# Optimization experiments

Hardware: AMD Instinct MI355X
Metric: run time of the kernel (lower is better)

Reference implementation:

```python
import math
import jax, jax.numpy as jnp
import numpy as np

K = 10          # hard-coded k in forward
ALPHA = 0.1
THETA = 0.5
BN_EPS = 1e-5


def setup_inputs() -> dict:
    key = jax.random.key(0)
    ks = jax.random.split(key, 8)
    B, N, H, L = 16, 4096, 128, 4
    s = lambda i, shp: jax.random.normal(ks[i], shp, jnp.float32) * 0.05
    return dict(
        pos=jax.random.normal(ks[0], (B, N, 3), jnp.float32),
        W0=s(1, (3, H)), b0=jnp.zeros((H,), jnp.float32),
        Wc=s(2, (L, H, H)),
        W1=s(3, (H, H)), b1=jnp.zeros((H,), jnp.float32),
        Wm1=s(4, (H, H)), bm1=jnp.zeros((H,), jnp.float32),
        g1=jnp.ones((H,), jnp.float32), be1=jnp.zeros((H,), jnp.float32),
        Wm2=s(5, (H, H)), bm2=jnp.zeros((H,), jnp.float32),
        g2=jnp.ones((H,), jnp.float32), be2=jnp.zeros((H,), jnp.float32),
        Wout=s(6, (H, 10)), bout=jnp.zeros((10,), jnp.float32),
    )


def _knn_idx(pos, k):
    # per-graph squared pairwise distances [B,N,N]; batch dim = graph id,
    # so no cross-graph edges (mirrors knn(x, x, k, batch, batch)).
    sq = jnp.sum(pos * pos, axis=-1)
    d2 = sq[:, :, None] + sq[:, None, :] - 2.0 * jnp.einsum('bnd,bmd->bnm', pos, pos)
    _, idx = jax.lax.top_k(-d2, k)  # [B,N,K], includes self (dist 0)
    return idx


def _bn_relu(x, g, b):
    # BatchNorm1d in training mode: batch statistics, biased variance
    mu = x.mean(0)
    var = x.var(0)
    return jax.nn.relu((x - mu) * jax.lax.rsqrt(var + BN_EPS) * g + b)


def _forward(pos, nbr, W0, b0, Wc, W1, b1, Wm1, bm1, g1, be1, Wm2, bm2, g2, be2, Wout, bout):
    x0 = jax.nn.relu(pos @ W0 + b0)                 # [B,N,H]
    x = x0
    gather = jax.vmap(lambda xb, nb: xb[nb])        # [B,N,K,H]
    for l in range(Wc.shape[0]):
        agg = gather(x, nbr).sum(axis=2)            # sum-aggregate, edge_weight = 1
        h = (1.0 - ALPHA) * agg + ALPHA * x0        # GCN2Conv initial residual
        beta = math.log(THETA / (l + 1) + 1.0)      # identity mapping strength
        x = jax.nn.relu((1.0 - beta) * h + beta * (h @ Wc[l]))
    x = x @ W1 + b1                                 # lins[1]
    pooled = x.max(axis=1)                          # global_max_pool -> [B,H]
    y = _bn_relu(pooled @ Wm1 + bm1, g1, be1)
    y = _bn_relu(y @ Wm2 + bm2, g2, be2)
    y = y @ Wout + bout
    return jax.nn.log_softmax(y, axis=-1)


def reference(pos, W0, b0, Wc, W1, b1, Wm1, bm1, g1, be1, Wm2, bm2, g2, be2, Wout, bout):
    nbr = _knn_idx(pos, K)  # index-only, non-differentiable (as in torch knn)
    return _forward(pos, nbr, W0, b0, Wc, W1, b1,
                    Wm1, bm1, g1, be1, Wm2, bm2, g2, be2, Wout, bout)
```

## Files before the change

kernel.cpp:

```cpp
#include <hip/hip_runtime.h>
#include <math.h>

#define NPTS 4096
#define HDIM 128
#define KNN 10
#define NSPLIT 4
#define CTILE 1024
#define SLOTS 12

__device__ __forceinline__ float relu_f(float x) { return x > 0.f ? x : 0.f; }
__device__ __forceinline__ float med3_f(float a, float b, float c) {
    return __builtin_amdgcn_fmed3f(a, b, c);
}

__global__ __launch_bounds__(256) void knn_part(const float* __restrict__ pos,
                                                uint2* __restrict__ pdi)
{
    __shared__ float4 spt[CTILE];
    const int bid = blockIdx.x;
    const int s = bid & 3;
    const int chunk = (bid >> 2) & 15;
    const int b = bid >> 6;
    const float* pb = pos + (size_t)b * NPTS * 3;
    const int c0 = s << 10;

    for (int j = threadIdx.x; j < CTILE; j += 256) {
        int g = c0 + j;
        float x = pb[3 * g + 0], y = pb[3 * g + 1], z = pb[3 * g + 2];
        float sq = __fadd_rn(__fadd_rn(__fmul_rn(x, x), __fmul_rn(y, y)), __fmul_rn(z, z));
        spt[j] = make_float4(x, y, z, sq);
    }
    __syncthreads();

    const int i = chunk * 256 + threadIdx.x;
    const float qx = pb[3 * i + 0], qy = pb[3 * i + 1], qz = pb[3 * i + 2];
    const float qw = __fadd_rn(__fadd_rn(__fmul_rn(qx, qx), __fmul_rn(qy, qy)), __fmul_rn(qz, qz));

    float bd[KNN];
#pragma unroll
    for (int m = 0; m < KNN; ++m) bd[m] = INFINITY;

#pragma unroll 4
    for (int j = 0; j < CTILE; ++j) {
        float4 p = spt[j];
        float dot = __fadd_rn(__fadd_rn(__fmul_rn(qx, p.x), __fmul_rn(qy, p.y)),
                              __fmul_rn(qz, p.z));
        float d2 = __fsub_rn(__fadd_rn(qw, p.w), __fmul_rn(2.f, dot));
#pragma unroll
        for (int m = KNN - 1; m > 0; --m) bd[m] = med3_f(d2, bd[m - 1], bd[m]);
        bd[0] = fminf(d2, bd[0]);
    }
    const float thr = bd[KNN - 1];

    uint2* o = pdi + ((size_t)(b * NPTS + i) * NSPLIT + s) * SLOTS;
    int cnt = 0;
#pragma unroll 4
    for (int j = 0; j < CTILE; ++j) {
        float4 p = spt[j];
        float dot = __fadd_rn(__fadd_rn(__fmul_rn(qx, p.x), __fmul_rn(qy, p.y)),
                              __fmul_rn(qz, p.z));
        float d2 = __fsub_rn(__fadd_rn(qw, p.w), __fmul_rn(2.f, dot));
        if (d2 <= thr && cnt < SLOTS) {
            o[cnt] = make_uint2(__float_as_uint(d2), (unsigned)(c0 + j));
            ++cnt;
        }
    }
}

__global__ __launch_bounds__(256) void knn_merge(const uint2* __restrict__ pdi,
                                                 int* __restrict__ nbr)
{
    const int q = blockIdx.x * 256 + threadIdx.x;
    const uint2* in = pdi + (size_t)q * (NSPLIT * SLOTS);
    float bd[KNN];
    int   bi[KNN];
#pragma unroll
    for (int m = 0; m < KNN; ++m) { bd[m] = 3.4e38f; bi[m] = 0; }
#pragma unroll
    for (int u = 0; u < NSPLIT * SLOTS; ++u) {
        uint2 v = in[u];
        float d2 = __uint_as_float(v.x);
        int   ix = (int)v.y;
        if (d2 < bd[KNN - 1]) {
            bool c[KNN];
#pragma unroll
            for (int m = 0; m < KNN; ++m) c[m] = d2 < bd[m];
#pragma unroll
            for (int m = KNN - 1; m > 0; --m) {
                bd[m] = c[m] ? (c[m - 1] ? bd[m - 1] : d2) : bd[m];
                bi[m] = c[m] ? (c[m - 1] ? bi[m - 1] : ix) : bi[m];
            }
            bd[0] = c[0] ? d2 : bd[0];
            bi[0] = c[0] ? ix : bi[0];
        }
    }
    const int b = q >> 12;
    int* o = nbr + (size_t)q * KNN;
#pragma unroll
    for (int m = 0; m < KNN; ++m) o[m] = (b << 12) + bi[m];
}

__global__ __launch_bounds__(256) void x0_kernel(const float* __restrict__ pos,
                                                 const float* __restrict__ W0,
                                                 const float* __restrict__ b0,
                                                 float* __restrict__ x0)
{
    int gid = blockIdx.x * 256 + threadIdx.x;
    int node = gid >> 5, qd = gid & 31;
    float px = pos[node * 3 + 0], py = pos[node * 3 + 1], pz = pos[node * 3 + 2];
    const float4 w0 = ((const float4*)W0)[qd];
    const float4 w1 = ((const float4*)W0)[32 + qd];
    const float4 w2 = ((const float4*)W0)[64 + qd];
    const float4 bb = ((const float4*)b0)[qd];
    float4 r;
    r.x = relu_f(fmaf(pz, w2.x, fmaf(py, w1.x, fmaf(px, w0.x, bb.x))));
    r.y = relu_f(fmaf(pz, w2.y, fmaf(py, w1.y, fmaf(px, w0.y, bb.y))));
    r.z = relu_f(fmaf(pz, w2.z, fmaf(py, w1.z, fmaf(px, w0.z, bb.z))));
    r.w = relu_f(fmaf(pz, w2.w, fmaf(py, w1.w, fmaf(px, w0.w, bb.w))));
    ((float4*)x0)[gid] = r;
}

__global__ __launch_bounds__(256) void gcn_layer(const float* __restrict__ xin,
                                                 float* __restrict__ xout,
                                                 const float* __restrict__ pos,
                                                 const float* __restrict__ W0,
                                                 const float* __restrict__ b0,
                                                 const float* __restrict__ Wl,
                                                 const int* __restrict__ nbr,
                                                 float omb, float beta)
{
    __shared__ float sh[64][129];
    __shared__ float sW[32 * 128];
    __shared__ float sW0[512];
    const int t = threadIdx.x;
    const int bid = blockIdx.x;
    const int swz = (bid & 7) * 128 + (bid >> 3);
    const int node0 = swz * 64;

    if (t < 128) {
        sW0[t] = W0[t]; sW0[128 + t] = W0[128 + t];
        sW0[256 + t] = W0[256 + t]; sW0[384 + t] = b0[t];
    }
    __syncthreads();

    const float4* xin4 = (const float4*)xin;
    for (int u = t; u < 64 * 32; u += 256) {
        int n = u >> 5, qd = u & 31;
        int node = node0 + n;
        float ax = 0.f, ay = 0.f, az = 0.f, aw = 0.f;
        const int* nb = nbr + node * KNN;
#pragma unroll
        for (int k = 0; k < KNN; ++k) {
            float4 v = xin4[nb[k] * 32 + qd];
            ax += v.x; ay += v.y; az += v.z; aw += v.w;
        }
        float px = pos[node * 3 + 0], py = pos[node * 3 + 1], pz = pos[node * 3 + 2];
        int c = qd * 4;
        sh[n][c + 0] = fmaf(0.9f, ax, 0.1f * relu_f(fmaf(pz, sW0[256 + c + 0], fmaf(py, sW0[128 + c + 0], fmaf(px, sW0[c + 0], sW0[384 + c + 0])))));
        sh[n][c + 1] = fmaf(0.9f, ay, 0.1f * relu_f(fmaf(pz, sW0[256 + c + 1], fmaf(py, sW0[128 + c + 1], fmaf(px, sW0[c + 1], sW0[384 + c + 1])))));
        sh[n][c + 2] = fmaf(0.9f, az, 0.1f * relu_f(fmaf(pz, sW0[256 + c + 2], fmaf(py, sW0[128 + c + 2], fmaf(px, sW0[c + 2], sW0[384 + c + 2])))));
        sh[n][c + 3] = fmaf(0.9f, aw, 0.1f * relu_f(fmaf(pz, sW0[256 + c + 3], fmaf(py, sW0[128 + c + 3], fmaf(px, sW0[c + 3], sW0[384 + c + 3])))));
    }

    const int rg = t >> 4;
    const int cq = t & 15;
    float acc[4][8];
#pragma unroll
    for (int r = 0; r < 4; ++r)
#pragma unroll
        for (int j = 0; j < 8; ++j) acc[r][j] = 0.f;

    const float4* W4 = (const float4*)Wl;
    for (int quarter = 0; quarter < 4; ++quarter) {
        __syncthreads();
        for (int u = t; u < 1024; u += 256) ((float4*)sW)[u] = W4[quarter * 1024 + u];
        __syncthreads();
#pragma unroll 4
        for (int ii = 0; ii < 32; ++ii) {
            int i = quarter * 32 + ii;
            float hv0 = sh[rg * 4 + 0][i];
            float hv1 = sh[rg * 4 + 1][i];
            float hv2 = sh[rg * 4 + 2][i];
            float hv3 = sh[rg * 4 + 3][i];
            const float4* row = (const float4*)(sW + ii * 128);
            float4 wA = row[cq];
            float4 wB = row[cq + 16];
            acc[0][0] = fmaf(hv0, wA.x, acc[0][0]); acc[0][1] = fmaf(hv0, wA.y, acc[0][1]);
            acc[0][2] = fmaf(hv0, wA.z, acc[0][2]); acc[0][3] = fmaf(hv0, wA.w, acc[0][3]);
            acc[0][4] = fmaf(hv0, wB.x, acc[0][4]); acc[0][5] = fmaf(hv0, wB.y, acc[0][5]);
            acc[0][6] = fmaf(hv0, wB.z, acc[0][6]); acc[0][7] = fmaf(hv0, wB.w, acc[0][7]);
            acc[1][0] = fmaf(hv1, wA.x, acc[1][0]); acc[1][1] = fmaf(hv1, wA.y, acc[1][1]);
            acc[1][2] = fmaf(hv1, wA.z, acc[1][2]); acc[1][3] = fmaf(hv1, wA.w, acc[1][3]);
            acc[1][4] = fmaf(hv1, wB.x, acc[1][4]); acc[1][5] = fmaf(hv1, wB.y, acc[1][5]);
            acc[1][6] = fmaf(hv1, wB.z, acc[1][6]); acc[1][7] = fmaf(hv1, wB.w, acc[1][7]);
            acc[2][0] = fmaf(hv2, wA.x, acc[2][0]); acc[2][1] = fmaf(hv2, wA.y, acc[2][1]);
            acc[2][2] = fmaf(hv2, wA.z, acc[2][2]); acc[2][3] = fmaf(hv2, wA.w, acc[2][3]);
            acc[2][4] = fmaf(hv2, wB.x, acc[2][4]); acc[2][5] = fmaf(hv2, wB.y, acc[2][5]);
            acc[2][6] = fmaf(hv2, wB.z, acc[2][6]); acc[2][7] = fmaf(hv2, wB.w, acc[2][7]);
            acc[3][0] = fmaf(hv3, wA.x, acc[3][0]); acc[3][1] = fmaf(hv3, wA.y, acc[3][1]);
            acc[3][2] = fmaf(hv3, wA.z, acc[3][2]); acc[3][3] = fmaf(hv3, wA.w, acc[3][3]);
            acc[3][4] = fmaf(hv3, wB.x, acc[3][4]); acc[3][5] = fmaf(hv3, wB.y, acc[3][5]);
            acc[3][6] = fmaf(hv3, wB.z, acc[3][6]); acc[3][7] = fmaf(hv3, wB.w, acc[3][7]);
        }
    }

#pragma unroll
    for (int r = 0; r < 4; ++r) {
        int row = rg * 4 + r;
        int node = node0 + row;
#pragma unroll
        for (int sel = 0; sel < 2; ++sel) {
            int c = cq * 4 + sel * 64;
            float4 o;
            o.x = relu_f(fmaf(omb, sh[row][c + 0], beta * acc[r][sel * 4 + 0]));
            o.y = relu_f(fmaf(omb, sh[row][c + 1], beta * acc[r][sel * 4 + 1]));
            o.z = relu_f(fmaf(omb, sh[row][c + 2], beta * acc[r][sel * 4 + 2]));
            o.w = relu_f(fmaf(omb, sh[row][c + 3], beta * acc[r][sel * 4 + 3]));
            ((float4*)(xout + (size_t)node * HDIM))[c >> 2] = o;
        }
    }
}

__global__ __launch_bounds__(256) void w1pool_kernel(const float* __restrict__ xin,
                                                     const float* __restrict__ W1,
                                                     const float* __restrict__ b1,
                                                     unsigned int* __restrict__ pool)
{
    __shared__ float sh[64][129];
    __shared__ float sW[32 * 128];
    __shared__ float smax[16][128];
    const int t = threadIdx.x;
    const int bid = blockIdx.x;
    const int swz = (bid & 7) * 128 + (bid >> 3);
    const int node0 = swz * 64;

    const float4* xin4 = (const float4*)xin;
    for (int u = t; u < 64 * 32; u += 256) {
        int n = u >> 5, qd = u & 31;
        float4 v = xin4[(node0 + n) * 32 + qd];
        int c = qd * 4;
        sh[n][c + 0] = v.x; sh[n][c + 1] = v.y; sh[n][c + 2] = v.z; sh[n][c + 3] = v.w;
    }

    const int rg = t >> 4;
    const int cq = t & 15;
    float acc[4][8];
#pragma unroll
    for (int r = 0; r < 4; ++r)
#pragma unroll
        for (int j = 0; j < 8; ++j) acc[r][j] = 0.f;

    const float4* W4 = (const float4*)W1;
    for (int quarter = 0; quarter < 4; ++quarter) {
        __syncthreads();
        for (int u = t; u < 1024; u += 256) ((float4*)sW)[u] = W4[quarter * 1024 + u];
        __syncthreads();
#pragma unroll 4
        for (int ii = 0; ii < 32; ++ii) {
            float hv0 = sh[rg * 4 + 0][quarter * 32 + ii];
            float hv1 = sh[rg * 4 + 1][quarter * 32 + ii];
            float hv2 = sh[rg * 4 + 2][quarter * 32 + ii];
            float hv3 = sh[rg * 4 + 3][quarter * 32 + ii];
            const float4* row = (const float4*)(sW + ii * 128);
            float4 wA = row[cq];
            float4 wB = row[cq + 16];
            acc[0][0] = fmaf(hv0, wA.x, acc[0][0]); acc[0][1] = fmaf(hv0, wA.y, acc[0][1]);
            acc[0][2] = fmaf(hv0, wA.z, acc[0][2]); acc[0][3] = fmaf(hv0, wA.w, acc[0][3]);
            acc[0][4] = fmaf(hv0, wB.x, acc[0][4]); acc[0][5] = fmaf(hv0, wB.y, acc[0][5]);
            acc[0][6] = fmaf(hv0, wB.z, acc[0][6]); acc[0][7] = fmaf(hv0, wB.w, acc[0][7]);
            acc[1][0] = fmaf(hv1, wA.x, acc[1][0]); acc[1][1] = fmaf(hv1, wA.y, acc[1][1]);
            acc[1][2] = fmaf(hv1, wA.z, acc[1][2]); acc[1][3] = fmaf(hv1, wA.w, acc[1][3]);
            acc[1][4] = fmaf(hv1, wB.x, acc[1][4]); acc[1][5] = fmaf(hv1, wB.y, acc[1][5]);
            acc[1][6] = fmaf(hv1, wB.z, acc[1][6]); acc[1][7] = fmaf(hv1, wB.w, acc[1][7]);
            acc[2][0] = fmaf(hv2, wA.x, acc[2][0]); acc[2][1] = fmaf(hv2, wA.y, acc[2][1]);
            acc[2][2] = fmaf(hv2, wA.z, acc[2][2]); acc[2][3] = fmaf(hv2, wA.w, acc[2][3]);
            acc[2][4] = fmaf(hv2, wB.x, acc[2][4]); acc[2][5] = fmaf(hv2, wB.y, acc[2][5]);
            acc[2][6] = fmaf(hv2, wB.z, acc[2][6]); acc[2][7] = fmaf(hv2, wB.w, acc[2][7]);
            acc[3][0] = fmaf(hv3, wA.x, acc[3][0]); acc[3][1] = fmaf(hv3, wA.y, acc[3][1]);
            acc[3][2] = fmaf(hv3, wA.z, acc[3][2]); acc[3][3] = fmaf(hv3, wA.w, acc[3][3]);
            acc[3][4] = fmaf(hv3, wB.x, acc[3][4]); acc[3][5] = fmaf(hv3, wB.y, acc[3][5]);
            acc[3][6] = fmaf(hv3, wB.z, acc[3][6]); acc[3][7] = fmaf(hv3, wB.w, acc[3][7]);
        }
    }

#pragma unroll
    for (int sel = 0; sel < 2; ++sel) {
#pragma unroll
        for (int j = 0; j < 4; ++j) {
            int c = cq * 4 + sel * 64 + j;
            float bc = b1[c];
            float m = acc[0][sel * 4 + j] + bc;
            m = fmaxf(m, acc[1][sel * 4 + j] + bc);
            m = fmaxf(m, acc[2][sel * 4 + j] + bc);
            m = fmaxf(m, acc[3][sel * 4 + j] + bc);
            smax[rg][c] = m;
        }
    }
    __syncthreads();
    if (t < 128) {
        float m = smax[0][t];
#pragma unroll
        for (int r = 1; r < 16; ++r) m = fmaxf(m, smax[r][t]);
        unsigned int u = __float_as_uint(m);
        unsigned int key = (u & 0x80000000u) ? ~u : (u | 0x80000000u);
        atomicMax(&pool[(node0 >> 12) * HDIM + t], key);
    }
}

__global__ __launch_bounds__(256) void head_kernel(const unsigned int* __restrict__ pool,
                                                   const float* __restrict__ Wm1, const float* __restrict__ bm1,
                                                   const float* __restrict__ g1,  const float* __restrict__ be1,
                                                   const float* __restrict__ Wm2, const float* __restrict__ bm2,
                                                   const float* __restrict__ g2,  const float* __restrict__ be2,
                                                   const float* __restrict__ Wout,const float* __restrict__ bout,
                                                   float* __restrict__ out)
{
    __shared__ float sA[16][128];
    __shared__ float sB[16][128];
    __shared__ float sL[16][10];
    const int t = threadIdx.x;
    for (int u = t; u < 2048; u += 256) {
        unsigned int k = pool[u];
        unsigned int orig = (k & 0x80000000u) ? (k ^ 0x80000000u) : ~k;
        sA[u >> 7][u & 127] = __uint_as_float(orig);
    }
    __syncthreads();

    if (t < 128) {
        float y[16];
#pragma unroll
        for (int b = 0; b < 16; ++b) y[b] = bm1[t];
        for (int i = 0; i < 128; ++i) {
            float w = Wm1[i * 128 + t];
#pragma unroll
            for (int b = 0; b < 16; ++b) y[b] = fmaf(sA[b][i], w, y[b]);
        }
        float mu = 0.f;
#pragma unroll
        for (int b = 0; b < 16; ++b) mu += y[b];
        mu *= (1.f / 16.f);
        float var = 0.f;
#pragma unroll
        for (int b = 0; b < 16; ++b) { float d = y[b] - mu; var = fmaf(d, d, var); }
        var *= (1.f / 16.f);
        float sc = g1[t] / sqrtf(var + 1e-5f);
        float sb = be1[t];
#pragma unroll
        for (int b = 0; b < 16; ++b) sB[b][t] = relu_f((y[b] - mu) * sc + sb);
    }
    __syncthreads();

    if (t < 128) {
        float y[16];
#pragma unroll
        for (int b = 0; b < 16; ++b) y[b] = bm2[t];
        for (int i = 0; i < 128; ++i) {
            float w = Wm2[i * 128 + t];
#pragma unroll
            for (int b = 0; b < 16; ++b) y[b] = fmaf(sB[b][i], w, y[b]);
        }
        float mu = 0.f;
#pragma unroll
        for (int b = 0; b < 16; ++b) mu += y[b];
        mu *= (1.f / 16.f);
        float var = 0.f;
#pragma unroll
        for (int b = 0; b < 16; ++b) { float d = y[b] - mu; var = fmaf(d, d, var); }
        var *= (1.f / 16.f);
        float sc = g2[t] / sqrtf(var + 1e-5f);
        float sb = be2[t];
#pragma unroll
        for (int b = 0; b < 16; ++b) sA[b][t] = relu_f((y[b] - mu) * sc + sb);
    }
    __syncthreads();

    if (t < 160) {
        int b = t / 10, o = t % 10;
        float a = bout[o];
        for (int i = 0; i < 128; ++i) a = fmaf(sA[b][i], Wout[i * 10 + o], a);
        sL[b][o] = a;
    }
    __syncthreads();

    if (t < 16) {
        float m = sL[t][0];
#pragma unroll
        for (int o = 1; o < 10; ++o) m = fmaxf(m, sL[t][o]);
        float s = 0.f;
#pragma unroll
        for (int o = 0; o < 10; ++o) s += expf(sL[t][o] - m);
        float ls = logf(s);
#pragma unroll
        for (int o = 0; o < 10; ++o) out[t * 10 + o] = sL[t][o] - m - ls;
    }
}

extern "C" void kernel_launch(void* const* d_in, const int* in_sizes, int n_in,
                              void* d_out, int out_size, void* d_ws, size_t ws_size,
                              hipStream_t stream)
{
    const float* pos = (const float*)d_in[0];
    const float* W0  = (const float*)d_in[1];
    const float* b0  = (const float*)d_in[2];
    const float* Wc  = (const float*)d_in[3];
    const float* W1  = (const float*)d_in[4];
    const float* b1  = (const float*)d_in[5];
    const float* Wm1 = (const float*)d_in[6];
    const float* bm1 = (const float*)d_in[7];
    const float* g1  = (const float*)d_in[8];
    const float* be1 = (const float*)d_in[9];
    const float* Wm2 = (const float*)d_in[10];
    const float* bm2 = (const float*)d_in[11];
    const float* g2  = (const float*)d_in[12];
    const float* be2 = (const float*)d_in[13];
    const float* Wout= (const float*)d_in[14];
    const float* bout= (const float*)d_in[15];
    float* out = (float*)d_out;

    char* ws = (char*)d_ws;
    float*        xA   = (float*)ws;
    float*        xB   = (float*)(ws + 33554432);
    int*          nbr  = (int*)(ws + 67108864);
    unsigned int* pool = (unsigned int*)(ws + 69730304);
    uint2* pdi = (uint2*)ws;

    hipMemsetAsync(pdi, 0xFF, (size_t)16 * NPTS * NSPLIT * SLOTS * 8, stream);
    knn_part<<<1024, 256, 0, stream>>>(pos, pdi);
    knn_merge<<<256, 256, 0, stream>>>(pdi, nbr);
    x0_kernel<<<8192, 256, 0, stream>>>(pos, W0, b0, xA);

    const float betas[4] = { 0.40546510810816438f, 0.22314355131420976f,
                             0.15415067982725836f, 0.11778303565638346f };
    gcn_layer<<<1024, 256, 0, stream>>>(xA, xB, pos, W0, b0, Wc + 0 * 16384, nbr, 1.f - betas[0], betas[0]);
    gcn_layer<<<1024, 256, 0, stream>>>(xB, xA, pos, W0, b0, Wc + 1 * 16384, nbr, 1.f - betas[1], betas[1]);
    gcn_layer<<<1024, 256, 0, stream>>>(xA, xB, pos, W0, b0, Wc + 2 * 16384, nbr, 1.f - betas[2], betas[2]);
    gcn_layer<<<1024, 256, 0, stream>>>(xB, xA, pos, W0, b0, Wc + 3 * 16384, nbr, 1.f - betas[3], betas[3]);

    hipMemsetAsync(pool, 0, 16 * HDIM * sizeof(unsigned int), stream);
    w1pool_kernel<<<1024, 256, 0, stream>>>(xA, W1, b1, pool);
    head_kernel<<<1, 256, 0, stream>>>(pool, Wm1, bm1, g1, be1, Wm2, bm2, g2, be2, Wout, bout, out);
}
```

Before: 602.2 us.

## Use split-bf16 MFMA for GCN layer and W1 pooling GEMMs

Replaces the scalar FP32 FMA inner products in gcn_layer and w1pool_kernel with MFMA 16x16x32 bf16 instructions. Both operands are split into high and low bf16 parts and combined with three MFMAs to approximate FP32 accuracy. A new wprep kernel pre-packs the weights into the MFMA fragment layout on every call. This cuts ALU time for the 128x128 GEMMs, but adds per-tile conversion of activations, extra LDS traffic for the split weights, and a small loss of precision.

```diff
diff --git a/kernel.cpp b/kernel.cpp
--- a/kernel.cpp
+++ b/kernel.cpp
@@ -8,9 +8,39 @@
 #define CTILE 1024
 #define SLOTS 12
 
+typedef __attribute__((ext_vector_type(4))) float f32x4;
+typedef __attribute__((ext_vector_type(4))) int   i32x4;
+typedef __attribute__((ext_vector_type(8))) short s16x8;
+
 __device__ __forceinline__ float relu_f(float x) { return x > 0.f ? x : 0.f; }
 __device__ __forceinline__ float med3_f(float a, float b, float c) {
     return __builtin_amdgcn_fmed3f(a, b, c);
+}
+__device__ __forceinline__ unsigned bf16_rne(float f) {
+    unsigned u = __float_as_uint(f);
+    return (u + 0x7fffu + ((u >> 16) & 1u)) >> 16;
+}
+__device__ __forceinline__ float bf2f(unsigned h) { return __uint_as_float(h << 16); }
+
+__global__ __launch_bounds__(256) void wprep(const float* __restrict__ Wc,
+                                             const float* __restrict__ W1,
+                                             unsigned* __restrict__ whi,
+                                             unsigned* __restrict__ wlo)
+{
+    const int m = blockIdx.x;
+    const float* W = (m < 4) ? (Wc + m * 16384) : W1;
+    unsigned* oh = whi + m * 8192;
+    unsigned* ol = wlo + m * 8192;
+    for (int u = threadIdx.x; u < 8192; u += 256) {
+        int kk = u >> 11, ct = (u >> 8) & 7, l = (u >> 2) & 63, d = u & 3;
+        int k0 = kk * 32 + ((l >> 4) << 3) + 2 * d;
+        int c  = ct * 16 + (l & 15);
+        float f0 = W[k0 * 128 + c], f1 = W[(k0 + 1) * 128 + c];
+        unsigned h0 = bf16_rne(f0), h1 = bf16_rne(f1);
+        float r0 = f0 - bf2f(h0), r1 = f1 - bf2f(h1);
+        oh[u] = h0 | (h1 << 16);
+        ol[u] = bf16_rne(r0) | (bf16_rne(r1) << 16);
+    }
 }
 
 __global__ __launch_bounds__(256) void knn_part(const float* __restrict__ pos,
@@ -120,17 +150,48 @@
     ((float4*)x0)[gid] = r;
 }
 
+__device__ __forceinline__ void gemm_kk(const float* shrow, const unsigned* sB,
+                                        int l, f32x4* acc)
+{
+    float f[8];
+#pragma unroll
+    for (int j = 0; j < 8; ++j) f[j] = shrow[j];
+    unsigned ah[4], al[4];
+#pragma unroll
+    for (int d = 0; d < 4; ++d) {
+        unsigned h0 = bf16_rne(f[2 * d]), h1 = bf16_rne(f[2 * d + 1]);
+        ah[d] = h0 | (h1 << 16);
+        float r0 = f[2 * d] - bf2f(h0), r1 = f[2 * d + 1] - bf2f(h1);
+        al[d] = bf16_rne(r0) | (bf16_rne(r1) << 16);
+    }
+    i32x4 ahv = { (int)ah[0], (int)ah[1], (int)ah[2], (int)ah[3] };
+    i32x4 alv = { (int)al[0], (int)al[1], (int)al[2], (int)al[3] };
+    s16x8 Ah = __builtin_bit_cast(s16x8, ahv);
+    s16x8 Al = __builtin_bit_cast(s16x8, alv);
+#pragma unroll
+    for (int ct = 0; ct < 8; ++ct) {
+        i32x4 bh = *(const i32x4*)&sB[(ct * 64 + l) * 4];
+        i32x4 bl = *(const i32x4*)&sB[2048 + (ct * 64 + l) * 4];
+        s16x8 Bh = __builtin_bit_cast(s16x8, bh);
+        s16x8 Bl = __builtin_bit_cast(s16x8, bl);
+        acc[ct] = __builtin_amdgcn_mfma_f32_16x16x32_bf16(Ah, Bh, acc[ct], 0, 0, 0);
+        acc[ct] = __builtin_amdgcn_mfma_f32_16x16x32_bf16(Al, Bh, acc[ct], 0, 0, 0);
+        acc[ct] = __builtin_amdgcn_mfma_f32_16x16x32_bf16(Ah, Bl, acc[ct], 0, 0, 0);
+    }
+}
+
 __global__ __launch_bounds__(256) void gcn_layer(const float* __restrict__ xin,
                                                  float* __restrict__ xout,
                                                  const float* __restrict__ pos,
                                                  const float* __restrict__ W0,
                                                  const float* __restrict__ b0,
-                                                 const float* __restrict__ Wl,
+                                                 const unsigned* __restrict__ whi,
+                                                 const unsigned* __restrict__ wlo,
                                                  const int* __restrict__ nbr,
                                                  float omb, float beta)
 {
     __shared__ float sh[64][129];
-    __shared__ float sW[32 * 128];
+    __shared__ __align__(16) unsigned sB[4096];
     __shared__ float sW0[512];
     const int t = threadIdx.x;
     const int bid = blockIdx.x;
@@ -162,72 +223,43 @@
         sh[n][c + 3] = fmaf(0.9f, aw, 0.1f * relu_f(fmaf(pz, sW0[256 + c + 3], fmaf(py, sW0[128 + c + 3], fmaf(px, sW0[c + 3], sW0[384 + c + 3])))));
     }
 
-    const int rg = t >> 4;
-    const int cq = t & 15;
-    float acc[4][8];
-#pragma unroll
-    for (int r = 0; r < 4; ++r)
-#pragma unroll
-        for (int j = 0; j < 8; ++j) acc[r][j] = 0.f;
-
-    const float4* W4 = (const float4*)Wl;
-    for (int quarter = 0; quarter < 4; ++quarter) {
+    const int w = t >> 6, l = t & 63, lr = l & 15, lg = l >> 4;
+    f32x4 acc[8];
+    const f32x4 z4 = { 0.f, 0.f, 0.f, 0.f };
+#pragma unroll
+    for (int ct = 0; ct < 8; ++ct) acc[ct] = z4;
+
+    for (int kk = 0; kk < 4; ++kk) {
         __syncthreads();
-        for (int u = t; u < 1024; u += 256) ((float4*)sW)[u] = W4[quarter * 1024 + u];
+        const uint4* srch = (const uint4*)(whi + kk * 2048);
+        const uint4* srcl = (const uint4*)(wlo + kk * 2048);
+        uint4* dst = (uint4*)sB;
+        dst[t] = srch[t];           dst[256 + t] = srch[256 + t];
+        dst[512 + t] = srcl[t];     dst[768 + t] = srcl[256 + t];
         __syncthreads();
-#pragma unroll 4
-        for (int ii = 0; ii < 32; ++ii) {
-            int i = quarter * 32 + ii;
-            float hv0 = sh[rg * 4 + 0][i];
-            float hv1 = sh[rg * 4 + 1][i];
-            float hv2 = sh[rg * 4 + 2][i];
-            float hv3 = sh[rg * 4 + 3][i];
-            const float4* row = (const float4*)(sW + ii * 128);
-            float4 wA = row[cq];
-            float4 wB = row[cq + 16];
-            acc[0][0] = fmaf(hv0, wA.x, acc[0][0]); acc[0][1] = fmaf(hv0, wA.y, acc[0][1]);
-            acc[0][2] = fmaf(hv0, wA.z, acc[0][2]); acc[0][3] = fmaf(hv0, wA.w, acc[0][3]);
-            acc[0][4] = fmaf(hv0, wB.x, acc[0][4]); acc[0][5] = fmaf(hv0, wB.y, acc[0][5]);
-            acc[0][6] = fmaf(hv0, wB.z, acc[0][6]); acc[0][7] = fmaf(hv0, wB.w, acc[0][7]);
-            acc[1][0] = fmaf(hv1, wA.x, acc[1][0]); acc[1][1] = fmaf(hv1, wA.y, acc[1][1]);
-            acc[1][2] = fmaf(hv1, wA.z, acc[1][2]); acc[1][3] = fmaf(hv1, wA.w, acc[1][3]);
-            acc[1][4] = fmaf(hv1, wB.x, acc[1][4]); acc[1][5] = fmaf(hv1, wB.y, acc[1][5]);
-            acc[1][6] = fmaf(hv1, wB.z, acc[1][6]); acc[1][7] = fmaf(hv1, wB.w, acc[1][7]);
-            acc[2][0] = fmaf(hv2, wA.x, acc[2][0]); acc[2][1] = fmaf(hv2, wA.y, acc[2][1]);
-            acc[2][2] = fmaf(hv2, wA.z, acc[2][2]); acc[2][3] = fmaf(hv2, wA.w, acc[2][3]);
-            acc[2][4] = fmaf(hv2, wB.x, acc[2][4]); acc[2][5] = fmaf(hv2, wB.y, acc[2][5]);
-            acc[2][6] = fmaf(hv2, wB.z, acc[2][6]); acc[2][7] = fmaf(hv2, wB.w, acc[2][7]);
-            acc[3][0] = fmaf(hv3, wA.x, acc[3][0]); acc[3][1] = fmaf(hv3, wA.y, acc[3][1]);
-            acc[3][2] = fmaf(hv3, wA.z, acc[3][2]); acc[3][3] = fmaf(hv3, wA.w, acc[3][3]);
-            acc[3][4] = fmaf(hv3, wB.x, acc[3][4]); acc[3][5] = fmaf(hv3, wB.y, acc[3][5]);
-            acc[3][6] = fmaf(hv3, wB.z, acc[3][6]); acc[3][7] = fmaf(hv3, wB.w, acc[3][7]);
-        }
-    }
-
-#pragma unroll
-    for (int r = 0; r < 4; ++r) {
-        int row = rg * 4 + r;
-        int node = node0 + row;
-#pragma unroll
-        for (int sel = 0; sel < 2; ++sel) {
-            int c = cq * 4 + sel * 64;
-            float4 o;
-            o.x = relu_f(fmaf(omb, sh[row][c + 0], beta * acc[r][sel * 4 + 0]));
-            o.y = relu_f(fmaf(omb, sh[row][c + 1], beta * acc[r][sel * 4 + 1]));
-            o.z = relu_f(fmaf(omb, sh[row][c + 2], beta * acc[r][sel * 4 + 2]));
-            o.w = relu_f(fmaf(omb, sh[row][c + 3], beta * acc[r][sel * 4 + 3]));
-            ((float4*)(xout + (size_t)node * HDIM))[c >> 2] = o;
+        gemm_kk(&sh[w * 16 + lr][kk * 32 + lg * 8], sB, l, acc);
+    }
+
+#pragma unroll
+    for (int ct = 0; ct < 8; ++ct) {
+        int col = ct * 16 + lr;
+#pragma unroll
+        for (int r = 0; r < 4; ++r) {
+            int rw = w * 16 + lg * 4 + r;
+            float h = sh[rw][col];
+            xout[(size_t)(node0 + rw) * HDIM + col] = relu_f(fmaf(omb, h, beta * acc[ct][r]));
         }
     }
 }
 
 __global__ __launch_bounds__(256) void w1pool_kernel(const float* __restrict__ xin,
-                                                     const float* __restrict__ W1,
+                                                     const unsigned* __restrict__ whi,
+                                                     const unsigned* __restrict__ wlo,
                                                      const float* __restrict__ b1,
                                                      unsigned int* __restrict__ pool)
 {
     __shared__ float sh[64][129];
-    __shared__ float sW[32 * 128];
+    __shared__ __align__(16) unsigned sB[4096];
     __shared__ float smax[16][128];
     const int t = threadIdx.x;
     const int bid = blockIdx.x;
@@ -242,59 +274,28 @@
         sh[n][c + 0] = v.x; sh[n][c + 1] = v.y; sh[n][c + 2] = v.z; sh[n][c + 3] = v.w;
     }
 
-    const int rg = t >> 4;
-    const int cq = t & 15;
-    float acc[4][8];
-#pragma unroll
-    for (int r = 0; r < 4; ++r)
-#pragma unroll
-        for (int j = 0; j < 8; ++j) acc[r][j] = 0.f;
-
-    const float4* W4 = (const float4*)W1;
-    for (int quarter = 0; quarter < 4; ++quarter) {
+    const int w = t >> 6, l = t & 63, lr = l & 15, lg = l >> 4;
+    f32x4 acc[8];
+    const f32x4 z4 = { 0.f, 0.f, 0.f, 0.f };
+#pragma unroll
+    for (int ct = 0; ct < 8; ++ct) acc[ct] = z4;
+
+    for (int kk = 0; kk < 4; ++kk) {
         __syncthreads();
-        for (int u = t; u < 1024; u += 256) ((float4*)sW)[u] = W4[quarter * 1024 + u];
+        const uint4* srch = (const uint4*)(whi + kk * 2048);
+        const uint4* srcl = (const uint4*)(wlo + kk * 2048);
+        uint4* dst = (uint4*)sB;
+        dst[t] = srch[t];           dst[256 + t] = srch[256 + t];
+        dst[512 + t] = srcl[t];     dst[768 + t] = srcl[256 + t];
         __syncthreads();
-#pragma unroll 4
-        for (int ii = 0; ii < 32; ++ii) {
-            float hv0 = sh[rg * 4 + 0][quarter * 32 + ii];
-            float hv1 = sh[rg * 4 + 1][quarter * 32 + ii];
-            float hv2 = sh[rg * 4 + 2][quarter * 32 + ii];
-            float hv3 = sh[rg * 4 + 3][quarter * 32 + ii];
-            const float4* row = (const float4*)(sW + ii * 128);
-            float4 wA = row[cq];
-            float4 wB = row[cq + 16];
-            acc[0][0] = fmaf(hv0, wA.x, acc[0][0]); acc[0][1] = fmaf(hv0, wA.y, acc[0][1]);
-            acc[0][2] = fmaf(hv0, wA.z, acc[0][2]); acc[0][3] = fmaf(hv0, wA.w, acc[0][3]);
-            acc[0][4] = fmaf(hv0, wB.x, acc[0][4]); acc[0][5] = fmaf(hv0, wB.y, acc[0][5]);
-            acc[0][6] = fmaf(hv0, wB.z, acc[0][6]); acc[0][7] = fmaf(hv0, wB.w, acc[0][7]);
-            acc[1][0] = fmaf(hv1, wA.x, acc[1][0]); acc[1][1] = fmaf(hv1, wA.y, acc[1][1]);
-            acc[1][2] = fmaf(hv1, wA.z, acc[1][2]); acc[1][3] = fmaf(hv1, wA.w, acc[1][3]);
-            acc[1][4] = fmaf(hv1, wB.x, acc[1][4]); acc[1][5] = fmaf(hv1, wB.y, acc[1][5]);
-            acc[1][6] = fmaf(hv1, wB.z, acc[1][6]); acc[1][7] = fmaf(hv1, wB.w, acc[1][7]);
-            acc[2][0] = fmaf(hv2, wA.x, acc[2][0]); acc[2][1] = fmaf(hv2, wA.y, acc[2][1]);
-            acc[2][2] = fmaf(hv2, wA.z, acc[2][2]); acc[2][3] = fmaf(hv2, wA.w, acc[2][3]);
-            acc[2][4] = fmaf(hv2, wB.x, acc[2][4]); acc[2][5] = fmaf(hv2, wB.y, acc[2][5]);
-            acc[2][6] = fmaf(hv2, wB.z, acc[2][6]); acc[2][7] = fmaf(hv2, wB.w, acc[2][7]);
-            acc[3][0] = fmaf(hv3, wA.x, acc[3][0]); acc[3][1] = fmaf(hv3, wA.y, acc[3][1]);
-            acc[3][2] = fmaf(hv3, wA.z, acc[3][2]); acc[3][3] = fmaf(hv3, wA.w, acc[3][3]);
-            acc[3][4] = fmaf(hv3, wB.x, acc[3][4]); acc[3][5] = fmaf(hv3, wB.y, acc[3][5]);
-            acc[3][6] = fmaf(hv3, wB.z, acc[3][6]); acc[3][7] = fmaf(hv3, wB.w, acc[3][7]);
-        }
-    }
-
-#pragma unroll
-    for (int sel = 0; sel < 2; ++sel) {
-#pragma unroll
-        for (int j = 0; j < 4; ++j) {
-            int c = cq * 4 + sel * 64 + j;
-            float bc = b1[c];
-            float m = acc[0][sel * 4 + j] + bc;
-            m = fmaxf(m, acc[1][sel * 4 + j] + bc);
-            m = fmaxf(m, acc[2][sel * 4 + j] + bc);
-            m = fmaxf(m, acc[3][sel * 4 + j] + bc);
-            smax[rg][c] = m;
-        }
+        gemm_kk(&sh[w * 16 + lr][kk * 32 + lg * 8], sB, l, acc);
+    }
+
+#pragma unroll
+    for (int ct = 0; ct < 8; ++ct) {
+        int col = ct * 16 + lr;
+        float m = fmaxf(fmaxf(acc[ct][0], acc[ct][1]), fmaxf(acc[ct][2], acc[ct][3]));
+        smax[w * 4 + lg][col] = m + b1[col];
     }
     __syncthreads();
     if (t < 128) {
@@ -316,7 +317,7 @@
                                                    float* __restrict__ out)
 {
     __shared__ float sA[16][128];
-    __shared__ float sB[16][128];
+    __shared__ float sB2[16][128];
     __shared__ float sL[16][10];
     const int t = threadIdx.x;
     for (int u = t; u < 2048; u += 256) {
@@ -346,7 +347,7 @@
         float sc = g1[t] / sqrtf(var + 1e-5f);
         float sb = be1[t];
 #pragma unroll
-        for (int b = 0; b < 16; ++b) sB[b][t] = relu_f((y[b] - mu) * sc + sb);
+        for (int b = 0; b < 16; ++b) sB2[b][t] = relu_f((y[b] - mu) * sc + sb);
     }
     __syncthreads();
 
@@ -357,7 +358,7 @@
         for (int i = 0; i < 128; ++i) {
             float w = Wm2[i * 128 + t];
 #pragma unroll
-            for (int b = 0; b < 16; ++b) y[b] = fmaf(sB[b][i], w, y[b]);
+            for (int b = 0; b < 16; ++b) y[b] = fmaf(sB2[b][i], w, y[b]);
         }
         float mu = 0.f;
 #pragma unroll
@@ -422,21 +423,24 @@
     float*        xB   = (float*)(ws + 33554432);
     int*          nbr  = (int*)(ws + 67108864);
     unsigned int* pool = (unsigned int*)(ws + 69730304);
+    unsigned*     whi  = (unsigned*)(ws + 69738496);
+    unsigned*     wlo  = (unsigned*)(ws + 69902336);
     uint2* pdi = (uint2*)ws;
 
     hipMemsetAsync(pdi, 0xFF, (size_t)16 * NPTS * NSPLIT * SLOTS * 8, stream);
+    wprep<<<5, 256, 0, stream>>>(Wc, W1, whi, wlo);
     knn_part<<<1024, 256, 0, stream>>>(pos, pdi);
     knn_merge<<<256, 256, 0, stream>>>(pdi, nbr);
     x0_kernel<<<8192, 256, 0, stream>>>(pos, W0, b0, xA);
 
     const float betas[4] = { 0.40546510810816438f, 0.22314355131420976f,
                              0.15415067982725836f, 0.11778303565638346f };
-    gcn_layer<<<1024, 256, 0, stream>>>(xA, xB, pos, W0, b0, Wc + 0 * 16384, nbr, 1.f - betas[0], betas[0]);
-    gcn_layer<<<1024, 256, 0, stream>>>(xB, xA, pos, W0, b0, Wc + 1 * 16384, nbr, 1.f - betas[1], betas[1]);
-    gcn_layer<<<1024, 256, 0, stream>>>(xA, xB, pos, W0, b0, Wc + 2 * 16384, nbr, 1.f - betas[2], betas[2]);
-    gcn_layer<<<1024, 256, 0, stream>>>(xB, xA, pos, W0, b0, Wc + 3 * 16384, nbr, 1.f - betas[3], betas[3]);
+    gcn_layer<<<1024, 256, 0, stream>>>(xA, xB, pos, W0, b0, whi + 0 * 8192, wlo + 0 * 8192, nbr, 1.f - betas[0], betas[0]);
+    gcn_layer<<<1024, 256, 0, stream>>>(xB, xA, pos, W0, b0, whi + 1 * 8192, wlo + 1 * 8192, nbr, 1.f - betas[1], betas[1]);
+    gcn_layer<<<1024, 256, 0, stream>>>(xA, xB, pos, W0, b0, whi + 2 * 8192, wlo + 2 * 8192, nbr, 1.f - betas[2], betas[2]);
+    gcn_layer<<<1024, 256, 0, stream>>>(xB, xA, pos, W0, b0, whi + 3 * 8192, wlo + 3 * 8192, nbr, 1.f - betas[3], betas[3]);
 
     hipMemsetAsync(pool, 0, 16 * HDIM * sizeof(unsigned int), stream);
-    w1pool_kernel<<<1024, 256, 0, stream>>>(xA, W1, b1, pool);
+    w1pool_kernel<<<1024, 256, 0, stream>>>(xA, whi + 4 * 8192, wlo + 4 * 8192, b1, pool);
     head_kernel<<<1, 256, 0, stream>>>(pool, Wm1, bm1, g1, be1, Wm2, bm2, g2, be2, Wout, bout, out);
 }
```

New measurement: 543.0 us. -9.8%, faster.
